# Performance work log

Hardware: AMD Instinct MI355X
Metric: run time of the kernel (lower is better)

The kernel has to match this reference:

```python
import jax, jax.numpy as jnp
import numpy as np

N = 8192      # nodes
E = 262144    # edges per graph (avg degree 32)
D_IN = 256
HID = 64
HEADS = 2
NEG_SLOPE = 0.2  # PyG GATConv leaky_relu slope


def _self_loops(ei, n):
    loop = jnp.arange(n, dtype=ei.dtype)
    return jnp.concatenate([ei[0], loop]), jnp.concatenate([ei[1], loop])


def gat_conv(x, src, dst, W, att_src, att_dst, b, concat):
    # PyG GATConv: h=[N,H,C]; alpha=softmax_dst(leaky_relu(a_s[src]+a_d[dst]))
    n = x.shape[0]
    H, C = att_src.shape
    h = (x @ W).reshape(n, H, C)
    a_s = (h * att_src).sum(-1)           # [N,H]
    a_d = (h * att_dst).sum(-1)           # [N,H]
    e = jax.nn.leaky_relu(a_s[src] + a_d[dst], NEG_SLOPE)  # [Etot,H]
    e = e - jax.ops.segment_max(e, dst, num_segments=n)[dst]
    e = jnp.exp(e)
    denom = jax.ops.segment_sum(e, dst, num_segments=n)[dst] + 1e-16
    alpha = e / denom                     # edge softmax per target node
    msg = h[src] * alpha[:, :, None]      # [Etot,H,C]
    out = jax.ops.segment_sum(msg, dst, num_segments=n)  # [N,H,C]
    out = out.reshape(n, H * C) if concat else out.mean(axis=1)
    return out + b


def gcn_conv(x, src, dst, W, b):
    # PyG GCNConv: D^{-1/2}(A+I)D^{-1/2} X W + b (self loops already appended)
    n = x.shape[0]
    h = x @ W
    deg = jax.ops.segment_sum(jnp.ones_like(src, jnp.float32), dst, num_segments=n)
    dinv = jax.lax.rsqrt(jnp.maximum(deg, 1.0))
    norm = dinv[src] * dinv[dst]          # [Etot]
    return jax.ops.segment_sum(h[src] * norm[:, None], dst, num_segments=n) + b


def cross_attn(q_in, kv_in, Wq, bq, Wk, bk, Wv, bv, Wo, bo, num_heads):
    n, d = q_in.shape
    hd = d // num_heads
    q = (q_in @ Wq + bq).reshape(n, num_heads, hd)
    k = (kv_in @ Wk + bk).reshape(n, num_heads, hd)
    v = (kv_in @ Wv + bv).reshape(n, num_heads, hd)
    scores = jnp.einsum('qhd,khd->hqk', q, k) / np.sqrt(hd).astype(np.float32)
    attn = jax.nn.softmax(scores, axis=-1)                 # [H,N,N]
    out = jnp.einsum('hqk,khd->qhd', attn, v).reshape(n, d) @ Wo + bo
    weights = attn.mean(axis=0)[None]                      # [1,N,N] avg heads (torch default)
    return out, weights


def setup_inputs():
    key = jax.random.key(0)
    ks = jax.random.split(key, 24)
    w = lambda k, s: jax.random.normal(k, s, jnp.float32) * 0.05
    inp = {
        'x': jax.random.normal(ks[0], (N, D_IN), jnp.float32),
        'edge_index_tkg': jax.random.randint(ks[1], (2, E), 0, N, jnp.int64 if jax.config.jax_enable_x64 else jnp.int32),
        'edge_index_ekg': jax.random.randint(ks[2], (2, E), 0, N, jnp.int64 if jax.config.jax_enable_x64 else jnp.int32),
        # GAT layer 1: heads=2, concat=True
        'gat1_W': w(ks[3], (D_IN, HEADS * HID)),
        'gat1_att_src': w(ks[4], (HEADS, HID)),
        'gat1_att_dst': w(ks[5], (HEADS, HID)),
        'gat1_b': jnp.zeros((HEADS * HID,), jnp.float32),
        # GAT layer 2: heads=1, concat=False
        'gat2_W': w(ks[6], (HEADS * HID, HID)),
        'gat2_att_src': w(ks[7], (1, HID)),
        'gat2_att_dst': w(ks[8], (1, HID)),
        'gat2_b': jnp.zeros((HID,), jnp.float32),
        # GCN layers
        'gcn1_W': w(ks[9], (D_IN, HID)),
        'gcn1_b': jnp.zeros((HID,), jnp.float32),
        'gcn2_W': w(ks[10], (HID, HID)),
        'gcn2_b': jnp.zeros((HID,), jnp.float32),
        # cross attention (hidden=64, 2 heads)
        'Wq': w(ks[11], (HID, HID)), 'bq': jnp.zeros((HID,), jnp.float32),
        'Wk': w(ks[12], (HID, HID)), 'bk': jnp.zeros((HID,), jnp.float32),
        'Wv': w(ks[13], (HID, HID)), 'bv': jnp.zeros((HID,), jnp.float32),
        'Wo': w(ks[14], (HID, HID)), 'bo': jnp.zeros((HID,), jnp.float32),
        # MLP head
        'fc1_W': w(ks[15], (2 * HID, HID)), 'fc1_b': jnp.zeros((HID,), jnp.float32),
        'fc2_W': w(ks[16], (HID, 1)), 'fc2_b': jnp.zeros((1,), jnp.float32),
    }
    return inp


def reference(x, edge_index_tkg, edge_index_ekg,
              gat1_W, gat1_att_src, gat1_att_dst, gat1_b,
              gat2_W, gat2_att_src, gat2_att_dst, gat2_b,
              gcn1_W, gcn1_b, gcn2_W, gcn2_b,
              Wq, bq, Wk, bk, Wv, bv, Wo, bo,
              fc1_W, fc1_b, fc2_W, fc2_b):
    n = x.shape[0]
    src_t, dst_t = _self_loops(edge_index_tkg, n)
    src_e, dst_e = _self_loops(edge_index_ekg, n)

    h_tkg = jax.nn.elu(gat_conv(x, src_t, dst_t, gat1_W, gat1_att_src, gat1_att_dst, gat1_b, True))
    h_tkg = jax.nn.elu(gat_conv(h_tkg, src_t, dst_t, gat2_W, gat2_att_src, gat2_att_dst, gat2_b, False))

    h_ekg = jax.nn.relu(gcn_conv(x, src_e, dst_e, gcn1_W, gcn1_b))
    h_ekg = jax.nn.relu(gcn_conv(h_ekg, src_e, dst_e, gcn2_W, gcn2_b))

    h_attn, attn_weights = cross_attn(h_tkg, h_ekg, Wq, bq, Wk, bk, Wv, bv, Wo, bo, HEADS)

    h_fused = jnp.concatenate([h_tkg, h_attn], axis=1)   # [N, 2*HID]
    pred = (jax.nn.relu(h_fused @ fc1_W + fc1_b) @ fc2_W + fc2_b).squeeze(-1)
    return pred, attn_weights
```

## Files before the change

kernel.cpp:

```cpp
#include <hip/hip_runtime.h>
#include <cstdint>
#include <cstddef>

#define NN 8192
#define EE 262144
#define ET 270336

using short8  = __attribute__((ext_vector_type(8))) short;
using floatx4 = __attribute__((ext_vector_type(4))) float;

__device__ __forceinline__ unsigned short f2bf(float f) {
  unsigned int u = __float_as_uint(f);
  u += 0x7fffu + ((u >> 16) & 1u);
  return (unsigned short)(u >> 16);
}

__global__ void edge_hist2_k(const int* __restrict__ ei_t, const int* __restrict__ ei_e,
                             int* __restrict__ cnt_t, int* __restrict__ cnt_e) {
  int idx = blockIdx.x * 256 + threadIdx.x;
  int g = idx >= ET;
  int e = g ? idx - ET : idx;
  const int* ei = g ? ei_e : ei_t;
  int* cnt = g ? cnt_e : cnt_t;
  int d = (e < EE) ? ei[EE + e] : (e - EE);
  atomicAdd(&cnt[d], 1);
}

__global__ void scan2_k(int* cnt_t, int* off_t, int* cnt_e, int* off_e) {
  int* cnt = blockIdx.x ? cnt_e : cnt_t;
  int* off = blockIdx.x ? off_e : off_t;
  __shared__ int s[1024];
  int t = threadIdx.x;
  int v[8]; int base = t * 8; int sum = 0;
  #pragma unroll
  for (int j = 0; j < 8; ++j) { v[j] = cnt[base + j]; sum += v[j]; }
  s[t] = sum; __syncthreads();
  for (int o = 1; o < 1024; o <<= 1) {
    int x = (t >= o) ? s[t - o] : 0;
    __syncthreads();
    s[t] += x;
    __syncthreads();
  }
  int excl = s[t] - sum;
  #pragma unroll
  for (int j = 0; j < 8; ++j) { off[base + j] = excl; cnt[base + j] = excl; excl += v[j]; }
  if (t == 1023) off[NN] = excl;
}

__global__ void edge_scatter2_k(const int* __restrict__ ei_t, const int* __restrict__ ei_e,
                                int* __restrict__ pos_t, int* __restrict__ pos_e,
                                int* __restrict__ srcs_t, int* __restrict__ srcs_e) {
  int idx = blockIdx.x * 256 + threadIdx.x;
  int g = idx >= ET;
  int e = g ? idx - ET : idx;
  const int* ei = g ? ei_e : ei_t;
  int* pos = g ? pos_e : pos_t;
  int* srcs = g ? srcs_e : srcs_t;
  int sv, d;
  if (e < EE) { sv = ei[e]; d = ei[EE + e]; } else { sv = d = e - EE; }
  int p = atomicAdd(&pos[d], 1);
  srcs[p] = sv;
}

__device__ __forceinline__ void gemm_core(const float* __restrict__ A, int lda, int K,
                                          const float* __restrict__ Bs, int row0, int col,
                                          float acc[8]) {
  #pragma unroll
  for (int r = 0; r < 8; ++r) acc[r] = 0.f;
  for (int k = 0; k < K; k += 4) {
    float b0 = Bs[(k + 0) * 32 + col], b1 = Bs[(k + 1) * 32 + col];
    float b2 = Bs[(k + 2) * 32 + col], b3 = Bs[(k + 3) * 32 + col];
    #pragma unroll
    for (int r = 0; r < 8; ++r) {
      const float4 a4 = *(const float4*)(A + (size_t)(row0 + r) * lda + k);
      acc[r] = fmaf(a4.x, b0, acc[r]);
      acc[r] = fmaf(a4.y, b1, acc[r]);
      acc[r] = fmaf(a4.z, b2, acc[r]);
      acc[r] = fmaf(a4.w, b3, acc[r]);
    }
  }
}

__global__ __launch_bounds__(256) void mm_x_k(const float* __restrict__ x,
    const float* __restrict__ Wgat, const float* __restrict__ Wgcn,
    const float* __restrict__ as_w, const float* __restrict__ ad_w,
    float* __restrict__ h1, float* __restrict__ hg1,
    float* __restrict__ a_s1, float* __restrict__ a_d1) {
  __shared__ float Bs[256 * 32];
  const int tid = threadIdx.x, by = blockIdx.y;
  const bool gat = by < 4;
  const int NC = gat ? 128 : 64;
  const int c0 = gat ? by * 32 : (by - 4) * 32;
  const float* B = gat ? Wgat : Wgcn;
  for (int idx = tid; idx < 256 * 32; idx += 256)
    Bs[idx] = B[(idx >> 5) * NC + c0 + (idx & 31)];
  __syncthreads();
  const int row0 = blockIdx.x * 64 + (tid >> 5) * 8;
  const int col = tid & 31;
  float acc[8];
  gemm_core(x, 256, 256, Bs, row0, col, acc);
  if (gat) {
    #pragma unroll
    for (int r = 0; r < 8; ++r) h1[(size_t)(row0 + r) * 128 + c0 + col] = acc[r];
    const int head = c0 >> 6;
    const float asw = as_w[head * 64 + (c0 & 63) + col];
    const float adw = ad_w[head * 64 + (c0 & 63) + col];
    float ps[8], pd[8];
    #pragma unroll
    for (int r = 0; r < 8; ++r) { ps[r] = acc[r] * asw; pd[r] = acc[r] * adw; }
    #pragma unroll
    for (int m = 16; m >= 1; m >>= 1)
      #pragma unroll
      for (int r = 0; r < 8; ++r) { ps[r] += __shfl_xor(ps[r], m); pd[r] += __shfl_xor(pd[r], m); }
    if (col == 0) {
      #pragma unroll
      for (int r = 0; r < 8; ++r) {
        atomicAdd(&a_s1[(row0 + r) * 2 + head], ps[r]);
        atomicAdd(&a_d1[(row0 + r) * 2 + head], pd[r]);
      }
    }
  } else {
    #pragma unroll
    for (int r = 0; r < 8; ++r) hg1[(size_t)(row0 + r) * 64 + c0 + col] = acc[r];
  }
}

template<int H, int C>
__device__ __forceinline__ void gat_agg_body(const float* __restrict__ h,
    const float* __restrict__ a_s, const float* __restrict__ a_d,
    const int* __restrict__ off, const int* __restrict__ srcs,
    const float* __restrict__ bias, float* __restrict__ out, int ldout, int b) {
  constexpr int HC = H * C;
  const int tid = threadIdx.x;
  const int hd = tid / C;
  const int r0 = off[b], r1 = off[b + 1];
  __shared__ int s_src[HC];
  __shared__ float s_w[HC][H];
  float ad[H];
  #pragma unroll
  for (int hh = 0; hh < H; ++hh) ad[hh] = a_d[b * H + hh];
  float acc = 0.f, den = 0.f;
  for (int base = r0; base < r1; base += HC) {
    __syncthreads();
    int e = base + tid;
    if (e < r1) {
      int sv = srcs[e];
      s_src[tid] = sv;
      #pragma unroll
      for (int hh = 0; hh < H; ++hh) {
        float xv = a_s[sv * H + hh] + ad[hh];
        xv = xv > 0.f ? xv : 0.2f * xv;
        s_w[tid][hh] = __expf(xv);
      }
    }
    __syncthreads();
    int cnt = min(HC, r1 - base);
    for (int j = 0; j < cnt; ++j) {
      float wv = s_w[j][hd];
      den += wv;
      acc = fmaf(wv, h[(size_t)s_src[j] * HC + tid], acc);
    }
  }
  float o = acc / den + bias[tid];
  out[(size_t)b * ldout + tid] = o > 0.f ? o : (__expf(o) - 1.f);
}

template<int H, int C>
__global__ void gat_agg_k(const float* __restrict__ h, const float* __restrict__ a_s,
                          const float* __restrict__ a_d, const int* __restrict__ off,
                          const int* __restrict__ srcs, const float* __restrict__ bias,
                          float* __restrict__ out, int ldout) {
  gat_agg_body<H, C>(h, a_s, a_d, off, srcs, bias, out, ldout, blockIdx.x);
}

__global__ __launch_bounds__(128) void agg1_k(
    const float* __restrict__ h1, const float* __restrict__ a_s1, const float* __restrict__ a_d1,
    const int* __restrict__ off_t, const int* __restrict__ src_t,
    const float* __restrict__ gat1_b, float* __restrict__ g1out,
    const float* __restrict__ hg1, const int* __restrict__ off_e, const int* __restrict__ src_e,
    const float* __restrict__ gcn1_b, const float* __restrict__ gcn2_W, float* __restrict__ h2g) {
  const int tid = threadIdx.x;
  if (blockIdx.x < NN) {
    gat_agg_body<2, 64>(h1, a_s1, a_d1, off_t, src_t, gat1_b, g1out, 128, blockIdx.x);
  } else {
    const int nb = (blockIdx.x - NN) * 2;
    const int sub = tid >> 6, t = tid & 63;
    const int node = nb + sub;
    __shared__ int s_src2[2][64];
    __shared__ float s_nrm2[2][64];
    __shared__ float s_row2[2][64];
    const int r0 = off_e[node], r1 = off_e[node + 1];
    const int cA = off_e[nb + 1] - off_e[nb];
    const int cB = off_e[nb + 2] - off_e[nb + 1];
    const int trips = (max(cA, cB) + 63) >> 6;
    float dinv_b = rsqrtf((float)max(r1 - r0, 1));
    float acc = 0.f;
    for (int it = 0; it < trips; ++it) {
      __syncthreads();
      int e = r0 + it * 64 + t;
      if (e < r1) {
        int sv = src_e[e];
        s_src2[sub][t] = sv;
        int ds = off_e[sv + 1] - off_e[sv];
        s_nrm2[sub][t] = dinv_b * rsqrtf((float)max(ds, 1));
      }
      __syncthreads();
      int cnt = min(64, r1 - (r0 + it * 64));
      for (int j = 0; j < cnt; ++j)
        acc = fmaf(s_nrm2[sub][j], hg1[(size_t)s_src2[sub][j] * 64 + t], acc);
    }
    s_row2[sub][t] = fmaxf(acc + gcn1_b[t], 0.f);
    __syncthreads();
    float acc2 = 0.f;
    for (int k = 0; k < 64; ++k)
      acc2 = fmaf(s_row2[sub][k], gcn2_W[k * 64 + t], acc2);
    h2g[(size_t)node * 64 + t] = acc2;
  }
}

__global__ __launch_bounds__(256) void mm2_k(
    const float* __restrict__ g1out, const float* __restrict__ gat2_W,
    const float* __restrict__ gat2_as, const float* __restrict__ gat2_ad,
    float* __restrict__ h2, float* __restrict__ a_s2, float* __restrict__ a_d2,
    const float* __restrict__ h2g, const int* __restrict__ off_e, const int* __restrict__ src_e,
    const float* __restrict__ gcn2_b, float* __restrict__ hekg) {
  const int tid = threadIdx.x;
  if (blockIdx.x < 256) {
    __shared__ float Bs[128 * 32];
    const int bx = blockIdx.x & 127;
    const int c0 = (blockIdx.x >> 7) * 32;
    for (int idx = tid; idx < 128 * 32; idx += 256)
      Bs[idx] = gat2_W[(idx >> 5) * 64 + c0 + (idx & 31)];
    __syncthreads();
    const int row0 = bx * 64 + (tid >> 5) * 8;
    const int col = tid & 31;
    float acc[8];
    gemm_core(g1out, 128, 128, Bs, row0, col, acc);
    const float asw = gat2_as[c0 + col];
    const float adw = gat2_ad[c0 + col];
    float ps[8], pd[8];
    #pragma unroll
    for (int r = 0; r < 8; ++r) {
      h2[(size_t)(row0 + r) * 64 + c0 + col] = acc[r];
      ps[r] = acc[r] * asw; pd[r] = acc[r] * adw;
    }
    #pragma unroll
    for (int m = 16; m >= 1; m >>= 1)
      #pragma unroll
      for (int r = 0; r < 8; ++r) { ps[r] += __shfl_xor(ps[r], m); pd[r] += __shfl_xor(pd[r], m); }
    if (col == 0) {
      #pragma unroll
      for (int r = 0; r < 8; ++r) {
        atomicAdd(&a_s2[row0 + r], ps[r]);
        atomicAdd(&a_d2[row0 + r], pd[r]);
      }
    }
  } else {
    const int nb = (blockIdx.x - 256) * 4;
    const int sub = tid >> 6, t = tid & 63;
    const int node = nb + sub;
    __shared__ int s_src4[4][64];
    __shared__ float s_nrm4[4][64];
    const int r0 = off_e[node], r1 = off_e[node + 1];
    int cmax = 0;
    #pragma unroll
    for (int i = 0; i < 4; ++i) cmax = max(cmax, off_e[nb + i + 1] - off_e[nb + i]);
    const int trips = (cmax + 63) >> 6;
    float dinv_b = rsqrtf((float)max(r1 - r0, 1));
    float acc = 0.f;
    for (int it = 0; it < trips; ++it) {
      __syncthreads();
      int e = r0 + it * 64 + t;
      if (e < r1) {
        int sv = src_e[e];
        s_src4[sub][t] = sv;
        int ds = off_e[sv + 1] - off_e[sv];
        s_nrm4[sub][t] = dinv_b * rsqrtf((float)max(ds, 1));
      }
      __syncthreads();
      int cnt = min(64, r1 - (r0 + it * 64));
      for (int j = 0; j < cnt; ++j)
        acc = fmaf(s_nrm4[sub][j], h2g[(size_t)s_src4[sub][j] * 64 + t], acc);
    }
    hekg[(size_t)node * 64 + t] = fmaxf(acc + gcn2_b[t], 0.f);
  }
}

__global__ __launch_bounds__(256) void mm_qkv_k(const float* __restrict__ htkg,
    const float* __restrict__ hekg,
    const float* __restrict__ Wq, const float* __restrict__ bq,
    const float* __restrict__ Wk, const float* __restrict__ bk,
    const float* __restrict__ Wv, const float* __restrict__ bv,
    unsigned short* __restrict__ qb, unsigned short* __restrict__ kb,
    unsigned short* __restrict__ Vt) {
  __shared__ float Bs[64 * 32];
  __shared__ float Ts[32][65];
  const int tid = threadIdx.x, by = blockIdx.y;
  const int kind = by >> 1;
  const int c0 = (by & 1) * 32;
  const float* A = (kind == 0) ? htkg : hekg;
  const float* B = (kind == 0) ? Wq : (kind == 1) ? Wk : Wv;
  const float* bias = (kind == 0) ? bq : (kind == 1) ? bk : bv;
  for (int idx = tid; idx < 64 * 32; idx += 256)
    Bs[idx] = B[(idx >> 5) * 64 + c0 + (idx & 31)];
  __syncthreads();
  const int row0 = blockIdx.x * 64 + (tid >> 5) * 8;
  const int col = tid & 31;
  float acc[8];
  gemm_core(A, 64, 64, Bs, row0, col, acc);
  const float bb = bias[c0 + col];
  if (kind == 0) {
    const float SCL = 0.17677669529663687f * 1.4426950408889634f;
    #pragma unroll
    for (int r = 0; r < 8; ++r)
      qb[(size_t)(row0 + r) * 64 + c0 + col] = f2bf((acc[r] + bb) * SCL);
  } else if (kind == 1) {
    #pragma unroll
    for (int r = 0; r < 8; ++r)
      kb[(size_t)(row0 + r) * 64 + c0 + col] = f2bf(acc[r] + bb);
  } else {
    const int rl = (tid >> 5) * 8;
    #pragma unroll
    for (int r = 0; r < 8; ++r) Ts[col][rl + r] = acc[r] + bb;
    __syncthreads();
    const int c = tid >> 3, rr = (tid & 7) * 8;
    short8 pk;
    #pragma unroll
    for (int j = 0; j < 8; ++j) pk[j] = (short)f2bf(Ts[c][rr + j]);
    *(short8*)(Vt + (size_t)(c0 + c) * NN + blockIdx.x * 64 + rr) = pk;
  }
}

__global__ __launch_bounds__(256) void att_lsum_k(
    const unsigned short* __restrict__ qb, const unsigned short* __restrict__ kb,
    float* __restrict__ lsum) {
  __shared__ float lsh[4][16][2];
  const int tid = threadIdx.x;
  const int lane = tid & 63, wv = tid >> 6;
  const int ql = lane & 15, quad = lane >> 4;
  const int qt0 = blockIdx.x * 16;
  const floatx4 zf = {0.f, 0.f, 0.f, 0.f};

  short8 qf[2];
  #pragma unroll
  for (int h = 0; h < 2; ++h)
    qf[h] = *(const short8*)(qb + (size_t)(qt0 + ql) * 64 + h * 32 + quad * 8);

  float lacc[2][4];
  #pragma unroll
  for (int h = 0; h < 2; ++h)
    #pragma unroll
    for (int r = 0; r < 4; ++r) lacc[h][r] = 0.f;
  int kbase = blockIdx.y * 2048 + wv * 512;
  for (int it = 0; it < 16; ++it, kbase += 32) {
    short8 kf[2][2];
    #pragma unroll
    for (int kt = 0; kt < 2; ++kt)
      #pragma unroll
      for (int h = 0; h < 2; ++h)
        kf[kt][h] = *(const short8*)(kb + (size_t)(kbase + kt * 16 + ql) * 64 + h * 32 + quad * 8);
    #pragma unroll
    for (int h = 0; h < 2; ++h)
      #pragma unroll
      for (int kt = 0; kt < 2; ++kt) {
        floatx4 s = __builtin_amdgcn_mfma_f32_16x16x32_bf16(qf[h], kf[kt][h], zf, 0, 0, 0);
        #pragma unroll
        for (int r = 0; r < 4; ++r) lacc[h][r] += __builtin_amdgcn_exp2f(s[r]);
      }
  }
  #pragma unroll
  for (int o = 8; o >= 1; o >>= 1)
    #pragma unroll
    for (int h = 0; h < 2; ++h)
      #pragma unroll
      for (int r = 0; r < 4; ++r)
        lacc[h][r] += __shfl_xor(lacc[h][r], o, 16);
  if (ql == 0) {
    #pragma unroll
    for (int h = 0; h < 2; ++h)
      #pragma unroll
      for (int r = 0; r < 4; ++r)
        lsh[wv][quad * 4 + r][h] = lacc[h][r];
  }
  __syncthreads();
  if (tid < 32) {
    const int row = tid >> 1, h = tid & 1;
    float s = lsh[0][row][h] + lsh[1][row][h] + lsh[2][row][h] + lsh[3][row][h];
    atomicAdd(&lsum[(qt0 + row) * 2 + h], s);
  }
}

__global__ __launch_bounds__(256) void att_pv_k(
    const unsigned short* __restrict__ qb, const unsigned short* __restrict__ kb,
    const unsigned short* __restrict__ Vt, const float* __restrict__ lsum,
    float* __restrict__ attn, float* __restrict__ O) {
  __shared__ __align__(16) float Esh[4][2][16 * 36];
  __shared__ float Osh[16 * 64];
  const int tid = threadIdx.x;
  const int lane = tid & 63, wv = tid >> 6;
  const int ql = lane & 15, quad = lane >> 4;
  const int qt0 = blockIdx.x * 16;
  const floatx4 zf = {0.f, 0.f, 0.f, 0.f};

  for (int idx = tid; idx < 16 * 64; idx += 256) Osh[idx] = 0.f;
  __syncthreads();

  short8 qf[2];
  #pragma unroll
  for (int h = 0; h < 2; ++h)
    qf[h] = *(const short8*)(qb + (size_t)(qt0 + ql) * 64 + h * 32 + quad * 8);

  float invl[2][4];
  #pragma unroll
  for (int h = 0; h < 2; ++h)
    #pragma unroll
    for (int r = 0; r < 4; ++r)
      invl[h][r] = 1.0f / lsum[(qt0 + quad * 4 + r) * 2 + h];

  floatx4 oacc[2][2];
  #pragma unroll
  for (int h = 0; h < 2; ++h)
    #pragma unroll
    for (int hf = 0; hf < 2; ++hf) oacc[h][hf] = zf;

  const int r8 = lane >> 3;
  const int c4 = (lane & 7) * 4;
  int kbase = blockIdx.y * 2048 + wv * 512;
  for (int it = 0; it < 16; ++it, kbase += 32) {
    short8 kf[2][2], vf[2][2];
    #pragma unroll
    for (int kt = 0; kt < 2; ++kt)
      #pragma unroll
      for (int h = 0; h < 2; ++h)
        kf[kt][h] = *(const short8*)(kb + (size_t)(kbase + kt * 16 + ql) * 64 + h * 32 + quad * 8);
    #pragma unroll
    for (int h = 0; h < 2; ++h)
      #pragma unroll
      for (int hf = 0; hf < 2; ++hf)
        vf[h][hf] = *(const short8*)(Vt + (size_t)(h * 32 + hf * 16 + ql) * NN + kbase + quad * 8);

    floatx4 p[2][2];
    #pragma unroll
    for (int h = 0; h < 2; ++h)
      #pragma unroll
      for (int kt = 0; kt < 2; ++kt) {
        floatx4 s = __builtin_amdgcn_mfma_f32_16x16x32_bf16(qf[h], kf[kt][h], zf, 0, 0, 0);
        #pragma unroll
        for (int r = 0; r < 4; ++r)
          p[h][kt][r] = __builtin_amdgcn_exp2f(s[r]) * invl[h][r];
      }
    #pragma unroll
    for (int h = 0; h < 2; ++h)
      #pragma unroll
      for (int kt = 0; kt < 2; ++kt)
        #pragma unroll
        for (int r = 0; r < 4; ++r)
          Esh[wv][h][(quad * 4 + r) * 36 + kt * 16 + ql] = p[h][kt][r];
    {
      const float4 a0 = *(const float4*)&Esh[wv][0][r8 * 36 + c4];
      const float4 b0 = *(const float4*)&Esh[wv][1][r8 * 36 + c4];
      const float4 a1 = *(const float4*)&Esh[wv][0][(r8 + 8) * 36 + c4];
      const float4 b1 = *(const float4*)&Esh[wv][1][(r8 + 8) * 36 + c4];
      float4 m0, m1;
      m0.x = 0.5f * (a0.x + b0.x); m0.y = 0.5f * (a0.y + b0.y);
      m0.z = 0.5f * (a0.z + b0.z); m0.w = 0.5f * (a0.w + b0.w);
      m1.x = 0.5f * (a1.x + b1.x); m1.y = 0.5f * (a1.y + b1.y);
      m1.z = 0.5f * (a1.z + b1.z); m1.w = 0.5f * (a1.w + b1.w);
      *(float4*)&attn[(size_t)(qt0 + r8) * NN + kbase + c4] = m0;
      *(float4*)&attn[(size_t)(qt0 + r8 + 8) * NN + kbase + c4] = m1;
    }
    #pragma unroll
    for (int h = 0; h < 2; ++h) {
      const float* ep = &Esh[wv][h][ql * 36 + quad * 8];
      float4 x0 = *(const float4*)ep;
      float4 x1 = *(const float4*)(ep + 4);
      short8 ef;
      ef[0] = (short)f2bf(x0.x); ef[1] = (short)f2bf(x0.y);
      ef[2] = (short)f2bf(x0.z); ef[3] = (short)f2bf(x0.w);
      ef[4] = (short)f2bf(x1.x); ef[5] = (short)f2bf(x1.y);
      ef[6] = (short)f2bf(x1.z); ef[7] = (short)f2bf(x1.w);
      #pragma unroll
      for (int hf = 0; hf < 2; ++hf)
        oacc[h][hf] = __builtin_amdgcn_mfma_f32_16x16x32_bf16(ef, vf[h][hf], oacc[h][hf], 0, 0, 0);
    }
  }
  #pragma unroll
  for (int h = 0; h < 2; ++h)
    #pragma unroll
    for (int hf = 0; hf < 2; ++hf)
      #pragma unroll
      for (int r = 0; r < 4; ++r)
        atomicAdd(&Osh[(quad * 4 + r) * 64 + h * 32 + hf * 16 + ql], oacc[h][hf][r]);
  __syncthreads();
  for (int idx = tid; idx < 16 * 64; idx += 256)
    atomicAdd(&O[(size_t)qt0 * 64 + idx], Osh[idx]);
}

__global__ __launch_bounds__(256) void tail_k(const float* __restrict__ O,
    const float* __restrict__ htkg, const float* __restrict__ Wo, const float* __restrict__ bo,
    const float* __restrict__ fc1W, const float* __restrict__ fc1b,
    const float* __restrict__ fc2W, const float* __restrict__ fc2b,
    float* __restrict__ pred) {
  __shared__ float Ws[8192];
  __shared__ float T1[2048];
  __shared__ float T2[2048];
  const int tid = threadIdx.x;
  const int col = tid & 63, rg = tid >> 6;
  const int rowbase = blockIdx.x * 32;
  for (int i = tid; i < 2048; i += 256) T1[i] = O[(size_t)rowbase * 64 + i];
  for (int i = tid; i < 4096; i += 256) Ws[i] = Wo[i];
  const float rbo = bo[col], rf1b = fc1b[col], rf2 = fc2W[col], rf2b = fc2b[0];
  __syncthreads();
  float ha[8];
  #pragma unroll
  for (int r = 0; r < 8; ++r) {
    const int row = rg * 8 + r;
    float acc = rbo;
    for (int k = 0; k < 64; ++k) acc = fmaf(T1[row * 64 + k], Ws[k * 64 + col], acc);
    ha[r] = acc;
  }
  __syncthreads();
  #pragma unroll
  for (int r = 0; r < 8; ++r) T2[(rg * 8 + r) * 64 + col] = ha[r];
  for (int i = tid; i < 2048; i += 256) T1[i] = htkg[(size_t)rowbase * 64 + i];
  for (int i = tid; i < 8192; i += 256) Ws[i] = fc1W[i];
  __syncthreads();
  #pragma unroll
  for (int r = 0; r < 8; ++r) {
    const int row = rg * 8 + r;
    float acc = rf1b;
    for (int k = 0; k < 64; ++k) acc = fmaf(T1[row * 64 + k], Ws[k * 64 + col], acc);
    for (int k = 0; k < 64; ++k) acc = fmaf(T2[row * 64 + k], Ws[(64 + k) * 64 + col], acc);
    float y = fmaxf(acc, 0.f);
    float v = y * rf2;
    #pragma unroll
    for (int m = 32; m >= 1; m >>= 1) v += __shfl_xor(v, m);
    if (col == 0) pred[rowbase + row] = v + rf2b;
  }
}

extern "C" void kernel_launch(void* const* d_in, const int* in_sizes, int n_in,
                              void* d_out, int out_size, void* d_ws, size_t ws_size,
                              hipStream_t stream) {
  (void)in_sizes; (void)n_in; (void)out_size; (void)ws_size;
  const float* x       = (const float*)d_in[0];
  const int*   ei_t    = (const int*)d_in[1];
  const int*   ei_e    = (const int*)d_in[2];
  const float* gat1_W  = (const float*)d_in[3];
  const float* gat1_as = (const float*)d_in[4];
  const float* gat1_ad = (const float*)d_in[5];
  const float* gat1_b  = (const float*)d_in[6];
  const float* gat2_W  = (const float*)d_in[7];
  const float* gat2_as = (const float*)d_in[8];
  const float* gat2_ad = (const float*)d_in[9];
  const float* gat2_b  = (const float*)d_in[10];
  const float* gcn1_W  = (const float*)d_in[11];
  const float* gcn1_b  = (const float*)d_in[12];
  const float* gcn2_W  = (const float*)d_in[13];
  const float* gcn2_b  = (const float*)d_in[14];
  const float* Wq = (const float*)d_in[15]; const float* bq = (const float*)d_in[16];
  const float* Wk = (const float*)d_in[17]; const float* bk = (const float*)d_in[18];
  const float* Wv = (const float*)d_in[19]; const float* bv = (const float*)d_in[20];
  const float* Wo = (const float*)d_in[21]; const float* bo = (const float*)d_in[22];
  const float* fc1_W = (const float*)d_in[23]; const float* fc1_b = (const float*)d_in[24];
  const float* fc2_W = (const float*)d_in[25]; const float* fc2_b = (const float*)d_in[26];

  float* out  = (float*)d_out;
  float* attn = out + NN;

  char* wsp = (char*)d_ws;
  size_t ofs = 0;
  auto take = [&](size_t bytes) -> char* {
    char* p = wsp + ofs;
    ofs = (ofs + bytes + 255) & ~(size_t)255;
    return p;
  };
  int*   pos_t = (int*)take(NN * 4);
  int*   pos_e = (int*)take(NN * 4);
  float* a_s1  = (float*)take((size_t)NN * 2 * 4);
  float* a_d1  = (float*)take((size_t)NN * 2 * 4);
  float* a_s2  = (float*)take((size_t)NN * 4);
  float* a_d2  = (float*)take((size_t)NN * 4);
  float* a_l   = (float*)take((size_t)NN * 2 * 4);
  float* Obuf  = (float*)take((size_t)NN * 64 * 4);
  const size_t zero_span = ofs;
  int* off_t = (int*)take((NN + 1) * 4);
  int* off_e = (int*)take((NN + 1) * 4);
  int* src_t = (int*)take((size_t)ET * 4);
  int* src_e = (int*)take((size_t)ET * 4);
  float* h1    = (float*)take((size_t)NN * 128 * 4);
  float* g1out = (float*)take((size_t)NN * 128 * 4);
  float* h2    = (float*)take((size_t)NN * 64 * 4);
  float* htkg  = (float*)take((size_t)NN * 64 * 4);
  float* hg1   = (float*)take((size_t)NN * 64 * 4);
  float* h2g   = (float*)take((size_t)NN * 64 * 4);
  float* hekg  = (float*)take((size_t)NN * 64 * 4);
  unsigned short* qb = (unsigned short*)take((size_t)NN * 64 * 2);
  unsigned short* kb = (unsigned short*)take((size_t)NN * 64 * 2);
  unsigned short* Vt = (unsigned short*)take((size_t)64 * NN * 2);

  hipMemsetAsync(wsp, 0, zero_span, stream);

  edge_hist2_k<<<2 * ET / 256, 256, 0, stream>>>(ei_t, ei_e, pos_t, pos_e);
  scan2_k<<<2, 1024, 0, stream>>>(pos_t, off_t, pos_e, off_e);
  edge_scatter2_k<<<2 * ET / 256, 256, 0, stream>>>(ei_t, ei_e, pos_t, pos_e, src_t, src_e);

  mm_x_k<<<dim3(128, 6), 256, 0, stream>>>(x, gat1_W, gcn1_W, gat1_as, gat1_ad,
                                           h1, hg1, a_s1, a_d1);
  agg1_k<<<NN + NN / 2, 128, 0, stream>>>(h1, a_s1, a_d1, off_t, src_t, gat1_b, g1out,
                                          hg1, off_e, src_e, gcn1_b, gcn2_W, h2g);
  mm2_k<<<256 + NN / 4, 256, 0, stream>>>(g1out, gat2_W, gat2_as, gat2_ad, h2, a_s2, a_d2,
                                          h2g, off_e, src_e, gcn2_b, hekg);
  gat_agg_k<1, 64><<<NN, 64, 0, stream>>>(h2, a_s2, a_d2, off_t, src_t, gat2_b, htkg, 64);

  mm_qkv_k<<<dim3(128, 6), 256, 0, stream>>>(htkg, hekg, Wq, bq, Wk, bk, Wv, bv, qb, kb, Vt);

  att_lsum_k<<<dim3(512, 4), 256, 0, stream>>>(qb, kb, a_l);
  att_pv_k<<<dim3(512, 4), 256, 0, stream>>>(qb, kb, Vt, a_l, attn, Obuf);

  tail_k<<<256, 256, 0, stream>>>(Obuf, htkg, Wo, bo, fc1_W, fc1_b, fc2_W, fc2_b, out);
}
```

Measured before the change: 702.5 us.

## Stage K/V tiles in swizzled LDS with double buffering for attention kernels

Both attention kernels now process larger query blocks (128 rows per block) and share K (and V) tiles across waves through double-buffered, XOR-swizzled LDS, prefetching the next tile into registers. This cuts redundant global K/V loads, which were previously done per wave for every 16-query tile. att_pv_k now uses 512 threads, writes the head-averaged attention weights directly from registers, and drops the shared O reduction in favour of per-wave global atomics. The cost is more LDS use, more syncthreads, and possibly less coalesced attn stores (16 floats per row segment).

```diff
diff --git a/kernel.cpp b/kernel.cpp
--- a/kernel.cpp
+++ b/kernel.cpp
@@ -334,166 +334,214 @@
 __global__ __launch_bounds__(256) void att_lsum_k(
     const unsigned short* __restrict__ qb, const unsigned short* __restrict__ kb,
     float* __restrict__ lsum) {
-  __shared__ float lsh[4][16][2];
+  __shared__ __align__(16) short Kbuf[2][64 * 64];
   const int tid = threadIdx.x;
   const int lane = tid & 63, wv = tid >> 6;
   const int ql = lane & 15, quad = lane >> 4;
-  const int qt0 = blockIdx.x * 16;
+  const int q0 = blockIdx.x * 128 + wv * 32;
+  const int k0 = blockIdx.y * 1024;
   const floatx4 zf = {0.f, 0.f, 0.f, 0.f};
 
-  short8 qf[2];
-  #pragma unroll
-  for (int h = 0; h < 2; ++h)
-    qf[h] = *(const short8*)(qb + (size_t)(qt0 + ql) * 64 + h * 32 + quad * 8);
-
-  float lacc[2][4];
-  #pragma unroll
-  for (int h = 0; h < 2; ++h)
-    #pragma unroll
-    for (int r = 0; r < 4; ++r) lacc[h][r] = 0.f;
-  int kbase = blockIdx.y * 2048 + wv * 512;
-  for (int it = 0; it < 16; ++it, kbase += 32) {
-    short8 kf[2][2];
-    #pragma unroll
-    for (int kt = 0; kt < 2; ++kt)
+  short8 qf[2][2];
+  #pragma unroll
+  for (int qt = 0; qt < 2; ++qt)
+    #pragma unroll
+    for (int h = 0; h < 2; ++h)
+      qf[qt][h] = *(const short8*)(qb + (size_t)(q0 + qt * 16 + ql) * 64 + h * 32 + quad * 8);
+
+  const int sr = tid >> 3, sc = tid & 7;
+  const int swc0 = (sc ^ (sr & 7)) * 8;
+  const int swc1 = (sc ^ ((sr + 32) & 7)) * 8;
+  short8 kr0, kr1;
+
+  float lacc[2][2][4];
+  #pragma unroll
+  for (int qt = 0; qt < 2; ++qt)
+    #pragma unroll
+    for (int h = 0; h < 2; ++h)
+      #pragma unroll
+      for (int r = 0; r < 4; ++r) lacc[qt][h][r] = 0.f;
+
+  {
+    const unsigned short* src = kb + (size_t)k0 * 64;
+    kr0 = *(const short8*)(src + sr * 64 + sc * 8);
+    kr1 = *(const short8*)(src + (sr + 32) * 64 + sc * 8);
+    *(short8*)&Kbuf[0][sr * 64 + swc0] = kr0;
+    *(short8*)&Kbuf[0][(sr + 32) * 64 + swc1] = kr1;
+  }
+  __syncthreads();
+
+  for (int t = 0; t < 16; ++t) {
+    if (t < 15) {
+      const unsigned short* src = kb + (size_t)(k0 + (t + 1) * 64) * 64;
+      kr0 = *(const short8*)(src + sr * 64 + sc * 8);
+      kr1 = *(const short8*)(src + (sr + 32) * 64 + sc * 8);
+    }
+    const short* Kc = Kbuf[t & 1];
+    #pragma unroll
+    for (int kt = 0; kt < 4; ++kt) {
+      const int row = kt * 16 + ql;
+      short8 kf[2];
       #pragma unroll
       for (int h = 0; h < 2; ++h)
-        kf[kt][h] = *(const short8*)(kb + (size_t)(kbase + kt * 16 + ql) * 64 + h * 32 + quad * 8);
-    #pragma unroll
-    for (int h = 0; h < 2; ++h)
-      #pragma unroll
-      for (int kt = 0; kt < 2; ++kt) {
-        floatx4 s = __builtin_amdgcn_mfma_f32_16x16x32_bf16(qf[h], kf[kt][h], zf, 0, 0, 0);
-        #pragma unroll
-        for (int r = 0; r < 4; ++r) lacc[h][r] += __builtin_amdgcn_exp2f(s[r]);
-      }
-  }
+        kf[h] = *(const short8*)&Kc[row * 64 + ((h * 4 + quad) ^ (row & 7)) * 8];
+      #pragma unroll
+      for (int qt = 0; qt < 2; ++qt)
+        #pragma unroll
+        for (int h = 0; h < 2; ++h) {
+          floatx4 s = __builtin_amdgcn_mfma_f32_16x16x32_bf16(qf[qt][h], kf[h], zf, 0, 0, 0);
+          #pragma unroll
+          for (int r = 0; r < 4; ++r) lacc[qt][h][r] += __builtin_amdgcn_exp2f(s[r]);
+        }
+    }
+    if (t < 15) {
+      *(short8*)&Kbuf[(t + 1) & 1][sr * 64 + swc0] = kr0;
+      *(short8*)&Kbuf[(t + 1) & 1][(sr + 32) * 64 + swc1] = kr1;
+    }
+    __syncthreads();
+  }
+
   #pragma unroll
   for (int o = 8; o >= 1; o >>= 1)
     #pragma unroll
-    for (int h = 0; h < 2; ++h)
-      #pragma unroll
-      for (int r = 0; r < 4; ++r)
-        lacc[h][r] += __shfl_xor(lacc[h][r], o, 16);
+    for (int qt = 0; qt < 2; ++qt)
+      #pragma unroll
+      for (int h = 0; h < 2; ++h)
+        #pragma unroll
+        for (int r = 0; r < 4; ++r)
+          lacc[qt][h][r] += __shfl_xor(lacc[qt][h][r], o, 16);
   if (ql == 0) {
     #pragma unroll
-    for (int h = 0; h < 2; ++h)
-      #pragma unroll
-      for (int r = 0; r < 4; ++r)
-        lsh[wv][quad * 4 + r][h] = lacc[h][r];
-  }
-  __syncthreads();
-  if (tid < 32) {
-    const int row = tid >> 1, h = tid & 1;
-    float s = lsh[0][row][h] + lsh[1][row][h] + lsh[2][row][h] + lsh[3][row][h];
-    atomicAdd(&lsum[(qt0 + row) * 2 + h], s);
-  }
-}
-
-__global__ __launch_bounds__(256) void att_pv_k(
+    for (int qt = 0; qt < 2; ++qt)
+      #pragma unroll
+      for (int h = 0; h < 2; ++h)
+        #pragma unroll
+        for (int r = 0; r < 4; ++r)
+          atomicAdd(&lsum[(q0 + qt * 16 + quad * 4 + r) * 2 + h], lacc[qt][h][r]);
+  }
+}
+
+__global__ __launch_bounds__(512, 4) void att_pv_k(
     const unsigned short* __restrict__ qb, const unsigned short* __restrict__ kb,
     const unsigned short* __restrict__ Vt, const float* __restrict__ lsum,
     float* __restrict__ attn, float* __restrict__ O) {
-  __shared__ __align__(16) float Esh[4][2][16 * 36];
-  __shared__ float Osh[16 * 64];
+  __shared__ __align__(16) short Kbuf[2][64 * 64];
+  __shared__ __align__(16) short Vbuf[2][64 * 64];
+  __shared__ __align__(16) float Esh[8][2][16 * 36];
   const int tid = threadIdx.x;
   const int lane = tid & 63, wv = tid >> 6;
   const int ql = lane & 15, quad = lane >> 4;
-  const int qt0 = blockIdx.x * 16;
+  const int q0 = blockIdx.x * 128 + wv * 16;
+  const int k0 = blockIdx.y * 1024;
   const floatx4 zf = {0.f, 0.f, 0.f, 0.f};
 
-  for (int idx = tid; idx < 16 * 64; idx += 256) Osh[idx] = 0.f;
+  short8 qf[2];
+  #pragma unroll
+  for (int h = 0; h < 2; ++h)
+    qf[h] = *(const short8*)(qb + (size_t)(q0 + ql) * 64 + h * 32 + quad * 8);
+
+  float invl[2][4];
+  #pragma unroll
+  for (int h = 0; h < 2; ++h)
+    #pragma unroll
+    for (int r = 0; r < 4; ++r)
+      invl[h][r] = 1.0f / lsum[(q0 + quad * 4 + r) * 2 + h];
+
+  const int sr = tid >> 3, sc = tid & 7;
+  const int swc = (sc ^ (sr & 7)) * 8;
+  short8 krg, vrg;
+
+  floatx4 oacc[2][2];
+  #pragma unroll
+  for (int h = 0; h < 2; ++h)
+    #pragma unroll
+    for (int hf = 0; hf < 2; ++hf) oacc[h][hf] = zf;
+
+  {
+    krg = *(const short8*)(kb + (size_t)(k0 + sr) * 64 + sc * 8);
+    vrg = *(const short8*)(Vt + (size_t)sr * NN + k0 + sc * 8);
+    *(short8*)&Kbuf[0][sr * 64 + swc] = krg;
+    *(short8*)&Vbuf[0][sr * 64 + swc] = vrg;
+  }
   __syncthreads();
 
-  short8 qf[2];
+  for (int t = 0; t < 16; ++t) {
+    if (t < 15) {
+      krg = *(const short8*)(kb + (size_t)(k0 + (t + 1) * 64 + sr) * 64 + sc * 8);
+      vrg = *(const short8*)(Vt + (size_t)sr * NN + k0 + (t + 1) * 64 + sc * 8);
+    }
+    const short* Kc = Kbuf[t & 1];
+    const short* Vc = Vbuf[t & 1];
+    #pragma unroll
+    for (int ks = 0; ks < 2; ++ks) {
+      short8 kf[2][2], vf[2][2];
+      #pragma unroll
+      for (int kt = 0; kt < 2; ++kt) {
+        const int row = ks * 32 + kt * 16 + ql;
+        #pragma unroll
+        for (int h = 0; h < 2; ++h)
+          kf[kt][h] = *(const short8*)&Kc[row * 64 + ((h * 4 + quad) ^ (row & 7)) * 8];
+      }
+      #pragma unroll
+      for (int h = 0; h < 2; ++h)
+        #pragma unroll
+        for (int hf = 0; hf < 2; ++hf) {
+          const int d = h * 32 + hf * 16 + ql;
+          vf[h][hf] = *(const short8*)&Vc[d * 64 + ((ks * 4 + quad) ^ (d & 7)) * 8];
+        }
+
+      floatx4 p[2][2];
+      #pragma unroll
+      for (int h = 0; h < 2; ++h)
+        #pragma unroll
+        for (int kt = 0; kt < 2; ++kt) {
+          floatx4 s = __builtin_amdgcn_mfma_f32_16x16x32_bf16(qf[h], kf[kt][h], zf, 0, 0, 0);
+          #pragma unroll
+          for (int r = 0; r < 4; ++r)
+            p[h][kt][r] = __builtin_amdgcn_exp2f(s[r]) * invl[h][r];
+        }
+      #pragma unroll
+      for (int kt = 0; kt < 2; ++kt)
+        #pragma unroll
+        for (int r = 0; r < 4; ++r)
+          attn[(size_t)(q0 + quad * 4 + r) * NN + k0 + t * 64 + ks * 32 + kt * 16 + ql] =
+              0.5f * (p[0][kt][r] + p[1][kt][r]);
+      #pragma unroll
+      for (int h = 0; h < 2; ++h)
+        #pragma unroll
+        for (int kt = 0; kt < 2; ++kt)
+          #pragma unroll
+          for (int r = 0; r < 4; ++r)
+            Esh[wv][h][(quad * 4 + r) * 36 + kt * 16 + ql] = p[h][kt][r];
+      #pragma unroll
+      for (int h = 0; h < 2; ++h) {
+        const float* ep = &Esh[wv][h][ql * 36 + quad * 8];
+        float4 x0 = *(const float4*)ep;
+        float4 x1 = *(const float4*)(ep + 4);
+        short8 ef;
+        ef[0] = (short)f2bf(x0.x); ef[1] = (short)f2bf(x0.y);
+        ef[2] = (short)f2bf(x0.z); ef[3] = (short)f2bf(x0.w);
+        ef[4] = (short)f2bf(x1.x); ef[5] = (short)f2bf(x1.y);
+        ef[6] = (short)f2bf(x1.z); ef[7] = (short)f2bf(x1.w);
+        #pragma unroll
+        for (int hf = 0; hf < 2; ++hf)
+          oacc[h][hf] = __builtin_amdgcn_mfma_f32_16x16x32_bf16(ef, vf[h][hf], oacc[h][hf], 0, 0, 0);
+      }
+    }
+    if (t < 15) {
+      *(short8*)&Kbuf[(t + 1) & 1][sr * 64 + swc] = krg;
+      *(short8*)&Vbuf[(t + 1) & 1][sr * 64 + swc] = vrg;
+    }
+    __syncthreads();
+  }
+
   #pragma unroll
   for (int h = 0; h < 2; ++h)
-    qf[h] = *(const short8*)(qb + (size_t)(qt0 + ql) * 64 + h * 32 + quad * 8);
-
-  float invl[2][4];
-  #pragma unroll
-  for (int h = 0; h < 2; ++h)
-    #pragma unroll
-    for (int r = 0; r < 4; ++r)
-      invl[h][r] = 1.0f / lsum[(qt0 + quad * 4 + r) * 2 + h];
-
-  floatx4 oacc[2][2];
-  #pragma unroll
-  for (int h = 0; h < 2; ++h)
-    #pragma unroll
-    for (int hf = 0; hf < 2; ++hf) oacc[h][hf] = zf;
-
-  const int r8 = lane >> 3;
-  const int c4 = (lane & 7) * 4;
-  int kbase = blockIdx.y * 2048 + wv * 512;
-  for (int it = 0; it < 16; ++it, kbase += 32) {
-    short8 kf[2][2], vf[2][2];
-    #pragma unroll
-    for (int kt = 0; kt < 2; ++kt)
-      #pragma unroll
-      for (int h = 0; h < 2; ++h)
-        kf[kt][h] = *(const short8*)(kb + (size_t)(kbase + kt * 16 + ql) * 64 + h * 32 + quad * 8);
-    #pragma unroll
-    for (int h = 0; h < 2; ++h)
-      #pragma unroll
-      for (int hf = 0; hf < 2; ++hf)
-        vf[h][hf] = *(const short8*)(Vt + (size_t)(h * 32 + hf * 16 + ql) * NN + kbase + quad * 8);
-
-    floatx4 p[2][2];
-    #pragma unroll
-    for (int h = 0; h < 2; ++h)
-      #pragma unroll
-      for (int kt = 0; kt < 2; ++kt) {
-        floatx4 s = __builtin_amdgcn_mfma_f32_16x16x32_bf16(qf[h], kf[kt][h], zf, 0, 0, 0);
-        #pragma unroll
-        for (int r = 0; r < 4; ++r)
-          p[h][kt][r] = __builtin_amdgcn_exp2f(s[r]) * invl[h][r];
-      }
-    #pragma unroll
-    for (int h = 0; h < 2; ++h)
-      #pragma unroll
-      for (int kt = 0; kt < 2; ++kt)
-        #pragma unroll
-        for (int r = 0; r < 4; ++r)
-          Esh[wv][h][(quad * 4 + r) * 36 + kt * 16 + ql] = p[h][kt][r];
-    {
-      const float4 a0 = *(const float4*)&Esh[wv][0][r8 * 36 + c4];
-      const float4 b0 = *(const float4*)&Esh[wv][1][r8 * 36 + c4];
-      const float4 a1 = *(const float4*)&Esh[wv][0][(r8 + 8) * 36 + c4];
-      const float4 b1 = *(const float4*)&Esh[wv][1][(r8 + 8) * 36 + c4];
-      float4 m0, m1;
-      m0.x = 0.5f * (a0.x + b0.x); m0.y = 0.5f * (a0.y + b0.y);
-      m0.z = 0.5f * (a0.z + b0.z); m0.w = 0.5f * (a0.w + b0.w);
-      m1.x = 0.5f * (a1.x + b1.x); m1.y = 0.5f * (a1.y + b1.y);
-      m1.z = 0.5f * (a1.z + b1.z); m1.w = 0.5f * (a1.w + b1.w);
-      *(float4*)&attn[(size_t)(qt0 + r8) * NN + kbase + c4] = m0;
-      *(float4*)&attn[(size_t)(qt0 + r8 + 8) * NN + kbase + c4] = m1;
-    }
-    #pragma unroll
-    for (int h = 0; h < 2; ++h) {
-      const float* ep = &Esh[wv][h][ql * 36 + quad * 8];
-      float4 x0 = *(const float4*)ep;
-      float4 x1 = *(const float4*)(ep + 4);
-      short8 ef;
-      ef[0] = (short)f2bf(x0.x); ef[1] = (short)f2bf(x0.y);
-      ef[2] = (short)f2bf(x0.z); ef[3] = (short)f2bf(x0.w);
-      ef[4] = (short)f2bf(x1.x); ef[5] = (short)f2bf(x1.y);
-      ef[6] = (short)f2bf(x1.z); ef[7] = (short)f2bf(x1.w);
-      #pragma unroll
-      for (int hf = 0; hf < 2; ++hf)
-        oacc[h][hf] = __builtin_amdgcn_mfma_f32_16x16x32_bf16(ef, vf[h][hf], oacc[h][hf], 0, 0, 0);
-    }
-  }
-  #pragma unroll
-  for (int h = 0; h < 2; ++h)
     #pragma unroll
     for (int hf = 0; hf < 2; ++hf)
       #pragma unroll
       for (int r = 0; r < 4; ++r)
-        atomicAdd(&Osh[(quad * 4 + r) * 64 + h * 32 + hf * 16 + ql], oacc[h][hf][r]);
-  __syncthreads();
-  for (int idx = tid; idx < 16 * 64; idx += 256)
-    atomicAdd(&O[(size_t)qt0 * 64 + idx], Osh[idx]);
+        atomicAdd(&O[(size_t)(q0 + quad * 4 + r) * 64 + h * 32 + hf * 16 + ql], oacc[h][hf][r]);
 }
 
 __global__ __launch_bounds__(256) void tail_k(const float* __restrict__ O,
@@ -615,8 +663,8 @@
 
   mm_qkv_k<<<dim3(128, 6), 256, 0, stream>>>(htkg, hekg, Wq, bq, Wk, bk, Wv, bv, qb, kb, Vt);
 
-  att_lsum_k<<<dim3(512, 4), 256, 0, stream>>>(qb, kb, a_l);
-  att_pv_k<<<dim3(512, 4), 256, 0, stream>>>(qb, kb, Vt, a_l, attn, Obuf);
+  att_lsum_k<<<dim3(64, 8), 256, 0, stream>>>(qb, kb, a_l);
+  att_pv_k<<<dim3(64, 8), 512, 0, stream>>>(qb, kb, Vt, a_l, attn, Obuf);
 
   tail_k<<<256, 256, 0, stream>>>(Obuf, htkg, Wo, bo, fc1_W, fc1_b, fc2_W, fc2_b, out);
 }
```

Measured after the change: 580.7 us. 17.3% less time.
